# Kernel tuning notes

Measured on AMD Instinct MI355X. Metric: run time of the kernel, lower is better.

The kernel has to match this reference:

```python
import jax, jax.numpy as jnp
import numpy as np

N_NODES = 50000
IN_CH, HID_CH, OUT_CH = 128, 128, 64
N_EDGES = 800000


def setup_inputs() -> dict:
    key = jax.random.key(0)
    k = jax.random.split(key, 6)
    x = jax.random.normal(k[0], (N_NODES, IN_CH), dtype=jnp.float32)
    edge_index = jax.random.randint(k[1], (2, N_EDGES), 0, N_NODES, dtype=jnp.int64)
    # Glorot-ish init for weights
    W1 = jax.random.normal(k[2], (IN_CH, HID_CH), dtype=jnp.float32) * (1.0 / np.sqrt(IN_CH))
    b1 = jnp.zeros((HID_CH,), dtype=jnp.float32)
    W2 = jax.random.normal(k[3], (HID_CH, OUT_CH), dtype=jnp.float32) * (1.0 / np.sqrt(HID_CH))
    b2 = jnp.zeros((OUT_CH,), dtype=jnp.float32)
    return {"x": x, "edge_index": edge_index, "W1": W1, "b1": b1, "W2": W2, "b2": b2}


def _gcn_conv(x, src, dst, W, b, n_nodes):
    """PyG GCNConv: linear, add self-loops, symmetric deg^-1/2 normalization, scatter-add."""
    h = x @ W  # [N, F_out]
    loop = jnp.arange(n_nodes, dtype=src.dtype)
    s = jnp.concatenate([src, loop])  # [E+N]
    d = jnp.concatenate([dst, loop])
    # in-degree on target nodes (including self-loops), edge weight = 1
    deg = jnp.zeros((n_nodes,), dtype=h.dtype).at[d].add(1.0)
    dinv = jnp.where(deg > 0, jax.lax.rsqrt(deg), 0.0)
    norm = dinv[s] * dinv[d]  # [E+N]
    msg = h[s] * norm[:, None]  # [E+N, F_out]
    out = jax.ops.segment_sum(msg, d, num_segments=n_nodes)
    return out + b


def reference(x, edge_index, W1, b1, W2, b2):
    src, dst = edge_index[0], edge_index[1]
    h = _gcn_conv(x, src, dst, W1, b1, N_NODES)
    h = jax.nn.relu(h)
    # dropout in eval mode -> identity
    out = _gcn_conv(h, src, dst, W2, b2, N_NODES)
    return out
```

## Files before the change

kernel.cpp:

```cpp
#include <hip/hip_runtime.h>

typedef __attribute__((ext_vector_type(8))) short bf16x8;
typedef __attribute__((ext_vector_type(4))) float f32x4;

constexpr int NN = 50000;
constexpr int NE = 800000;
constexpr int C1 = 128;
constexpr int C2 = 64;
constexpr int NBK = 196;
constexpr int EPB = 2048;
constexpr int NBLK = (NE + EPB - 1) / EPB;
constexpr int MT = NN / 16;
constexpr int CAP = 8192;
constexpr int GB = (NN + 3) / 4;
constexpr int MMB = 500;
constexpr int MMWAVES = MMB * 4;

constexpr int K1G = 1024;
constexpr int MM1_NW = (K1G - NBLK) * 4;

__device__ __forceinline__ unsigned short f2bf(float f) {
    unsigned int u = __float_as_uint(f);
    u += 0x7FFFu + ((u >> 16) & 1u);
    return (unsigned short)(u >> 16);
}
__device__ __forceinline__ float2 bf2f(unsigned int u) {
    return make_float2(__uint_as_float(u << 16), __uint_as_float(u & 0xFFFF0000u));
}
__device__ __forceinline__ unsigned int pk2(float a, float b) {
    return (unsigned int)f2bf(a) | ((unsigned int)f2bf(b) << 16);
}
__device__ __forceinline__ bf16x8 pack8(float4 a, float4 b) {
    bf16x8 r;
    r[0] = (short)f2bf(a.x); r[1] = (short)f2bf(a.y);
    r[2] = (short)f2bf(a.z); r[3] = (short)f2bf(a.w);
    r[4] = (short)f2bf(b.x); r[5] = (short)f2bf(b.y);
    r[6] = (short)f2bf(b.z); r[7] = (short)f2bf(b.w);
    return r;
}

struct BinSmem {
    int lhist[NBK];
    int ls[256];
    int lcur[NBK];
    unsigned int lbuf[EPB];
};

__device__ void bin_work(const int* __restrict__ src, const int* __restrict__ dst,
                         unsigned int* __restrict__ ebuf, int* __restrict__ localOff,
                         BinSmem& S) {
    const int t = threadIdx.x;
    const int base = blockIdx.x * EPB;
    if (t < NBK) S.lhist[t] = 0;
    __syncthreads();
    int b[8]; unsigned int p[8];
    #pragma unroll
    for (int i = 0; i < 8; i++) {
        int e = base + i * 256 + t;
        if (e < NE) {
            int s = src[e], d = dst[e];
            b[i] = d >> 8;
            p[i] = ((unsigned int)(d & 255) << 16) | (unsigned int)s;
            atomicAdd(&S.lhist[b[i]], 1);
        } else b[i] = -1;
    }
    __syncthreads();
    int v = (t < NBK) ? S.lhist[t] : 0;
    S.ls[t] = v;
    __syncthreads();
    #pragma unroll
    for (int d = 1; d < 256; d <<= 1) {
        int u = (t >= d) ? S.ls[t - d] : 0;
        __syncthreads();
        S.ls[t] += u;
        __syncthreads();
    }
    if (t < NBK) {
        S.lcur[t] = S.ls[t] - v;
        localOff[blockIdx.x * 200 + t] = S.ls[t] - v;
    }
    if (t == NBK - 1) localOff[blockIdx.x * 200 + NBK] = S.ls[t];
    __syncthreads();
    #pragma unroll
    for (int i = 0; i < 8; i++) {
        if (b[i] >= 0) {
            int lp = atomicAdd(&S.lcur[b[i]], 1);
            S.lbuf[lp] = p[i];
        }
    }
    __syncthreads();
    #pragma unroll
    for (int i = 0; i < 8; i++)
        ebuf[base + i * 256 + t] = S.lbuf[i * 256 + t];
}

__device__ void mm1_work(const float* __restrict__ x, const float* __restrict__ W,
                         unsigned short* __restrict__ g1,
                         unsigned short (&wl)[4][8][64][8]) {
    const int t = threadIdx.x;
    for (int i = 0; i < 64; i++) {
        int idx = i * 256 + t;
        int k = idx >> 7, n = idx & 127;
        wl[k >> 5][n >> 4][((k >> 3) & 3) * 16 + (n & 15)][k & 7] = f2bf(W[idx]);
    }
    __syncthreads();
    const int lane = t & 63, lm = lane & 15, quad = lane >> 4;

    bf16x8 bfr[4][8];
    #pragma unroll
    for (int s = 0; s < 4; s++)
        #pragma unroll
        for (int nt = 0; nt < 8; nt++)
            bfr[s][nt] = *(const bf16x8*)&wl[s][nt][lane][0];

    const int widx = (blockIdx.x - NBLK) * 4 + (t >> 6);
    for (int tile = widx; tile < MT; tile += MM1_NW) {
        int row0 = tile << 4;
        const float* xr = x + (size_t)(row0 + lm) * 128 + quad * 8;
        bf16x8 af[4];
        #pragma unroll
        for (int s = 0; s < 4; s++) {
            float4 p = *(const float4*)(xr + s * 32);
            float4 q = *(const float4*)(xr + s * 32 + 4);
            af[s] = pack8(p, q);
        }
        f32x4 acc[8];
        #pragma unroll
        for (int nt = 0; nt < 8; nt++) acc[nt] = (f32x4){0.f, 0.f, 0.f, 0.f};
        #pragma unroll
        for (int s = 0; s < 4; s++)
            #pragma unroll
            for (int nt = 0; nt < 8; nt++)
                acc[nt] = __builtin_amdgcn_mfma_f32_16x16x32_bf16(af[s], bfr[s][nt],
                                                                  acc[nt], 0, 0, 0);
        #pragma unroll
        for (int nt = 0; nt < 8; nt++)
            #pragma unroll
            for (int r = 0; r < 4; r++)
                g1[(size_t)(row0 + quad * 4 + r) * 128 + nt * 16 + lm] = f2bf(acc[nt][r]);
    }
}

__global__ __launch_bounds__(256, 2) void k1_kernel(const int* __restrict__ src,
                                                    const int* __restrict__ dst,
                                                    unsigned int* __restrict__ ebuf,
                                                    int* __restrict__ localOff,
                                                    const float* __restrict__ x,
                                                    const float* __restrict__ W1,
                                                    unsigned short* __restrict__ g1) {
    __shared__ union { BinSmem b; unsigned short wl[4][8][64][8]; } sm;
    if (blockIdx.x < NBLK) bin_work(src, dst, ebuf, localOff, sm.b);
    else                   mm1_work(x, W1, g1, sm.wl);
}

__global__ __launch_bounds__(256) void place_kernel(const unsigned int* __restrict__ ebuf,
                                                    const int* __restrict__ localOff,
                                                    unsigned short* __restrict__ esrc,
                                                    int* __restrict__ cnt,
                                                    int* __restrict__ off,
                                                    float* __restrict__ dinv) {
    __shared__ unsigned int lbuf[CAP];
    __shared__ int lhist[256];
    __shared__ int ls[256];
    __shared__ int lcur[256];
    __shared__ int red[256];
    const int t = threadIdx.x;
    const int bkt = blockIdx.x;
    const int node0 = bkt << 8;
    const int nnodes = min(256, NN - node0);

    const int j0 = 2 * t, j1 = 2 * t + 1;
    int s0 = 0, l0 = 0, s1 = 0, l1 = 0;
    if (j0 < NBLK) { s0 = localOff[j0 * 200 + bkt]; l0 = localOff[j0 * 200 + bkt + 1] - s0; }
    if (j1 < NBLK) { s1 = localOff[j1 * 200 + bkt]; l1 = localOff[j1 * 200 + bkt + 1] - s1; }

    red[t] = s0 + s1;
    ls[t] = l0 + l1;
    lhist[t] = 0;
    __syncthreads();
    #pragma unroll
    for (int d = 1; d < 256; d <<= 1) {
        int u = (t >= d) ? ls[t - d] : 0;
        int r = (t + d < 256) ? red[t + d] : 0;
        __syncthreads();
        ls[t] += u;
        red[t] += r;
        __syncthreads();
    }
    const int segBase = red[0];
    const int total = ls[255];
    const int base0 = ls[t] - (l0 + l1);
    const int base1 = base0 + l0;
    const bool fits = (total <= CAP);

    if (fits) {
        const unsigned int* q0 = ebuf + j0 * EPB + s0;
        for (int k = 0; k < l0; k++) lbuf[base0 + k] = q0[k];
        const unsigned int* q1 = ebuf + j1 * EPB + s1;
        for (int k = 0; k < l1; k++) lbuf[base1 + k] = q1[k];
        __syncthreads();
        for (int k = t; k < total; k += 256) atomicAdd(&lhist[lbuf[k] >> 16], 1);
    } else {
        const unsigned int* q0 = ebuf + j0 * EPB + s0;
        for (int k = 0; k < l0; k++) atomicAdd(&lhist[q0[k] >> 16], 1);
        const unsigned int* q1 = ebuf + j1 * EPB + s1;
        for (int k = 0; k < l1; k++) atomicAdd(&lhist[q1[k] >> 16], 1);
    }
    __syncthreads();
    int v = lhist[t];
    ls[t] = v;
    __syncthreads();
    #pragma unroll
    for (int d = 1; d < 256; d <<= 1) {
        int u = (t >= d) ? ls[t - d] : 0;
        __syncthreads();
        ls[t] += u;
        __syncthreads();
    }
    int ex = ls[t] - v;
    lcur[t] = ex;
    if (t < nnodes) {
        cnt[node0 + t] = v;
        off[node0 + t] = segBase + ex;
        dinv[node0 + t] = rsqrtf((float)v + 1.0f);
    }
    __syncthreads();
    if (fits) {
        for (int k = t; k < total; k += 256) {
            unsigned int pp = lbuf[k];
            int lp = atomicAdd(&lcur[pp >> 16], 1);
            esrc[segBase + lp] = (unsigned short)(pp & 0xFFFFu);
        }
    } else {
        const unsigned int* q0 = ebuf + j0 * EPB + s0;
        for (int k = 0; k < l0; k++) {
            unsigned int pp = q0[k];
            int lp = atomicAdd(&lcur[pp >> 16], 1);
            esrc[segBase + lp] = (unsigned short)(pp & 0xFFFFu);
        }
        const unsigned int* q1 = ebuf + j1 * EPB + s1;
        for (int k = 0; k < l1; k++) {
            unsigned int pp = q1[k];
            int lp = atomicAdd(&lcur[pp >> 16], 1);
            esrc[segBase + lp] = (unsigned short)(pp & 0xFFFFu);
        }
    }
}

__global__ __launch_bounds__(256) void gather1_kernel(const unsigned short* __restrict__ g1,
                                                      const unsigned short* __restrict__ esrc,
                                                      const int* __restrict__ off,
                                                      const int* __restrict__ cnt,
                                                      const float* __restrict__ dinv,
                                                      const float* __restrict__ b1,
                                                      unsigned short* __restrict__ x2) {
    const int n = blockIdx.x * 4 + (threadIdx.x >> 6);
    if (n >= NN) return;
    const int lane = threadIdx.x & 63;
    const unsigned int* G = (const unsigned int*)g1;
    const float dn = dinv[n];
    float2 ps = bf2f(G[(size_t)n * 64 + lane]);
    float a0 = dn * ps.x, a1 = dn * ps.y;
    float c0 = 0.f, c1 = 0.f;
    const int s0 = off[n], c = cnt[n];
    for (int base = 0; base < c; base += 64) {
        const int m = min(64, c - base);
        int vidx = 0; float vdin = 0.f;
        if (lane < m) {
            vidx = esrc[s0 + base + lane];
            vdin = dinv[vidx];
        }
        int i = 0;
        for (; i + 3 < m; i += 4) {
            int sA = __shfl(vidx, i),     sB = __shfl(vidx, i + 1);
            int sC = __shfl(vidx, i + 2), sD = __shfl(vidx, i + 3);
            float dA = __shfl(vdin, i),     dB = __shfl(vdin, i + 1);
            float dC = __shfl(vdin, i + 2), dD = __shfl(vdin, i + 3);
            unsigned int vA = G[(size_t)sA * 64 + lane];
            unsigned int vB = G[(size_t)sB * 64 + lane];
            unsigned int vC = G[(size_t)sC * 64 + lane];
            unsigned int vD = G[(size_t)sD * 64 + lane];
            float2 pA = bf2f(vA); a0 = fmaf(dA, pA.x, a0); a1 = fmaf(dA, pA.y, a1);
            float2 pB = bf2f(vB); c0 = fmaf(dB, pB.x, c0); c1 = fmaf(dB, pB.y, c1);
            float2 pC = bf2f(vC); a0 = fmaf(dC, pC.x, a0); a1 = fmaf(dC, pC.y, a1);
            float2 pD = bf2f(vD); c0 = fmaf(dD, pD.x, c0); c1 = fmaf(dD, pD.y, c1);
        }
        for (; i < m; i++) {
            int sA = __shfl(vidx, i);
            float dA = __shfl(vdin, i);
            float2 pA = bf2f(G[(size_t)sA * 64 + lane]);
            a0 = fmaf(dA, pA.x, a0); a1 = fmaf(dA, pA.y, a1);
        }
    }
    a0 += c0; a1 += c1;
    const float2 bb = ((const float2*)b1)[lane];
    const float o0 = fmaxf(dn * a0 + bb.x, 0.f);
    const float o1 = fmaxf(dn * a1 + bb.y, 0.f);
    ((unsigned int*)x2)[(size_t)n * 64 + lane] = pk2(o0, o1);
}

__global__ __launch_bounds__(256, 2) void mm2_kernel(const unsigned short* __restrict__ x2,
                                                     const float* __restrict__ W,
                                                     const float* __restrict__ dinv,
                                                     unsigned short* __restrict__ g2) {
    __shared__ unsigned short wl[4][4][64][8];
    const int t = threadIdx.x;
    for (int i = 0; i < 32; i++) {
        int idx = i * 256 + t;
        int k = idx >> 6, n = idx & 63;
        wl[k >> 5][n >> 4][((k >> 3) & 3) * 16 + (n & 15)][k & 7] = f2bf(W[idx]);
    }
    __syncthreads();
    const int lane = t & 63, lm = lane & 15, quad = lane >> 4;

    bf16x8 bfr[4][4];
    #pragma unroll
    for (int s = 0; s < 4; s++)
        #pragma unroll
        for (int nt = 0; nt < 4; nt++)
            bfr[s][nt] = *(const bf16x8*)&wl[s][nt][lane][0];

    int wg = blockIdx.x * 4 + (t >> 6);
    for (int tile = wg; tile < MT; tile += MMWAVES) {
        int row0 = tile << 4;
        const bf16x8* xr = (const bf16x8*)(x2 + (size_t)(row0 + lm) * 128 + quad * 8);
        bf16x8 af[4];
        #pragma unroll
        for (int s = 0; s < 4; s++) af[s] = xr[s * 4];
        f32x4 acc[4];
        #pragma unroll
        for (int nt = 0; nt < 4; nt++) acc[nt] = (f32x4){0.f, 0.f, 0.f, 0.f};
        #pragma unroll
        for (int s = 0; s < 4; s++)
            #pragma unroll
            for (int nt = 0; nt < 4; nt++)
                acc[nt] = __builtin_amdgcn_mfma_f32_16x16x32_bf16(af[s], bfr[s][nt],
                                                                  acc[nt], 0, 0, 0);
        float4 dv = *(const float4*)(dinv + row0 + quad * 4);
        float dvv[4] = {dv.x, dv.y, dv.z, dv.w};
        #pragma unroll
        for (int nt = 0; nt < 4; nt++)
            #pragma unroll
            for (int r = 0; r < 4; r++)
                g2[(size_t)(row0 + quad * 4 + r) * 64 + nt * 16 + lm] =
                    f2bf(acc[nt][r] * dvv[r]);
    }
}

__global__ __launch_bounds__(256) void gather2_kernel(const unsigned short* __restrict__ g2,
                                                      const unsigned short* __restrict__ esrc,
                                                      const int* __restrict__ off,
                                                      const int* __restrict__ cnt,
                                                      const float* __restrict__ dinv,
                                                      const float* __restrict__ b2,
                                                      float* __restrict__ out) {
    const int n = blockIdx.x * 4 + (threadIdx.x >> 6);
    if (n >= NN) return;
    const int lane = threadIdx.x & 63;
    const unsigned short* G = g2;
    float a0 = __uint_as_float((unsigned int)G[(size_t)n * 64 + lane] << 16);
    float c0 = 0.f;
    const int s0 = off[n], c = cnt[n];
    for (int base = 0; base < c; base += 64) {
        const int m = min(64, c - base);
        int vidx = 0;
        if (lane < m) vidx = esrc[s0 + base + lane];
        int i = 0;
        for (; i + 3 < m; i += 4) {
            int sA = __shfl(vidx, i),     sB = __shfl(vidx, i + 1);
            int sC = __shfl(vidx, i + 2), sD = __shfl(vidx, i + 3);
            unsigned short vA = G[(size_t)sA * 64 + lane];
            unsigned short vB = G[(size_t)sB * 64 + lane];
            unsigned short vC = G[(size_t)sC * 64 + lane];
            unsigned short vD = G[(size_t)sD * 64 + lane];
            a0 += __uint_as_float((unsigned int)vA << 16);
            c0 += __uint_as_float((unsigned int)vB << 16);
            a0 += __uint_as_float((unsigned int)vC << 16);
            c0 += __uint_as_float((unsigned int)vD << 16);
        }
        for (; i < m; i++) {
            int sA = __shfl(vidx, i);
            a0 += __uint_as_float((unsigned int)G[(size_t)sA * 64 + lane] << 16);
        }
    }
    a0 += c0;
    out[(size_t)n * 64 + lane] = dinv[n] * a0 + b2[lane];
}

extern "C" void kernel_launch(void* const* d_in, const int* in_sizes, int n_in,
                              void* d_out, int out_size, void* d_ws, size_t ws_size,
                              hipStream_t stream) {
    const float* x  = (const float*)d_in[0];
    const int* edges = (const int*)d_in[1];
    const float* W1 = (const float*)d_in[2];
    const float* b1 = (const float*)d_in[3];
    const float* W2 = (const float*)d_in[4];
    const float* b2 = (const float*)d_in[5];
    const int* src = edges;
    const int* dst = edges + NE;

    int* localOff  = (int*)d_ws;
    unsigned int* ebuf = (unsigned int*)(localOff + 78208);
    unsigned short* esrc = (unsigned short*)(ebuf + (size_t)NBLK * EPB);
    int* cnt       = (int*)(esrc + 800768);
    int* off       = cnt + 50048;
    float* dinv    = (float*)(off + 50048);
    unsigned short* g1 = (unsigned short*)(dinv + 50048);
    unsigned short* x2 = g1 + (size_t)NN * C1;
    unsigned short* g2 = g1;
    float* out = (float*)d_out;

    k1_kernel<<<K1G, 256, 0, stream>>>(src, dst, ebuf, localOff, x, W1, g1);
    place_kernel<<<NBK, 256, 0, stream>>>(ebuf, localOff, esrc, cnt, off, dinv);
    gather1_kernel<<<GB, 256, 0, stream>>>(g1, esrc, off, cnt, dinv, b1, x2);
    mm2_kernel<<<MMB, 256, 0, stream>>>(x2, W2, dinv, g2);
    gather2_kernel<<<GB, 256, 0, stream>>>(g2, esrc, off, cnt, dinv, b2, out);
}
```

Baseline: 179.6 us.

## Split first GEMM across binning and placement kernels to overlap work

The first dense matmul (x@W1) is split into two tile ranges. The first 500 row tiles run alongside edge binning in k1, and the rest run alongside the placement/CSR build in a new fused k2 kernel. The k1 grid shrinks and the place kernel gains extra matmul blocks. The aim is to hide the single-bucket placement phase, which occupies only 196 blocks, behind useful GEMM work. The cost is load-balance risk across the two phases and a larger shared-memory union in k2, which may lower occupancy.

```diff
diff --git a/kernel.cpp b/kernel.cpp
--- a/kernel.cpp
+++ b/kernel.cpp
@@ -16,8 +16,11 @@
 constexpr int MMB = 500;
 constexpr int MMWAVES = MMB * 4;
 
-constexpr int K1G = 1024;
-constexpr int MM1_NW = (K1G - NBLK) * 4;
+constexpr int T1 = 500;
+constexpr int K1G = 512;
+constexpr int MM1_NW_A = (K1G - NBLK) * 4;
+constexpr int K2G = 853;
+constexpr int MM1_NW_B = (K2G - NBK) * 4;
 
 __device__ __forceinline__ unsigned short f2bf(float f) {
     unsigned int u = __float_as_uint(f);
@@ -44,6 +47,13 @@
     int ls[256];
     int lcur[NBK];
     unsigned int lbuf[EPB];
+};
+struct PlaceSmem {
+    unsigned int lbuf[CAP];
+    int lhist[256];
+    int ls[256];
+    int lcur[256];
+    int red[256];
 };
 
 __device__ void bin_work(const int* __restrict__ src, const int* __restrict__ dst,
@@ -96,7 +106,8 @@
 
 __device__ void mm1_work(const float* __restrict__ x, const float* __restrict__ W,
                          unsigned short* __restrict__ g1,
-                         unsigned short (&wl)[4][8][64][8]) {
+                         unsigned short (&wl)[4][8][64][8],
+                         int mblk, int nwaves, int tile0, int tile1) {
     const int t = threadIdx.x;
     for (int i = 0; i < 64; i++) {
         int idx = i * 256 + t;
@@ -113,8 +124,8 @@
         for (int nt = 0; nt < 8; nt++)
             bfr[s][nt] = *(const bf16x8*)&wl[s][nt][lane][0];
 
-    const int widx = (blockIdx.x - NBLK) * 4 + (t >> 6);
-    for (int tile = widx; tile < MT; tile += MM1_NW) {
+    const int widx = mblk * 4 + (t >> 6);
+    for (int tile = tile0 + widx; tile < tile1; tile += nwaves) {
         int row0 = tile << 4;
         const float* xr = x + (size_t)(row0 + lm) * 128 + quad * 8;
         bf16x8 af[4];
@@ -138,6 +149,96 @@
             #pragma unroll
             for (int r = 0; r < 4; r++)
                 g1[(size_t)(row0 + quad * 4 + r) * 128 + nt * 16 + lm] = f2bf(acc[nt][r]);
+    }
+}
+
+__device__ void place_work(const unsigned int* __restrict__ ebuf,
+                           const int* __restrict__ localOff,
+                           unsigned short* __restrict__ esrc,
+                           int* __restrict__ cnt,
+                           int* __restrict__ off,
+                           float* __restrict__ dinv,
+                           PlaceSmem& S) {
+    const int t = threadIdx.x;
+    const int bkt = blockIdx.x;
+    const int node0 = bkt << 8;
+    const int nnodes = min(256, NN - node0);
+
+    const int j0 = 2 * t, j1 = 2 * t + 1;
+    int s0 = 0, l0 = 0, s1 = 0, l1 = 0;
+    if (j0 < NBLK) { s0 = localOff[j0 * 200 + bkt]; l0 = localOff[j0 * 200 + bkt + 1] - s0; }
+    if (j1 < NBLK) { s1 = localOff[j1 * 200 + bkt]; l1 = localOff[j1 * 200 + bkt + 1] - s1; }
+
+    S.red[t] = s0 + s1;
+    S.ls[t] = l0 + l1;
+    S.lhist[t] = 0;
+    __syncthreads();
+    #pragma unroll
+    for (int d = 1; d < 256; d <<= 1) {
+        int u = (t >= d) ? S.ls[t - d] : 0;
+        int r = (t + d < 256) ? S.red[t + d] : 0;
+        __syncthreads();
+        S.ls[t] += u;
+        S.red[t] += r;
+        __syncthreads();
+    }
+    const int segBase = S.red[0];
+    const int total = S.ls[255];
+    const int base0 = S.ls[t] - (l0 + l1);
+    const int base1 = base0 + l0;
+    const bool fits = (total <= CAP);
+
+    if (fits) {
+        const unsigned int* q0 = ebuf + j0 * EPB + s0;
+        for (int k = 0; k < l0; k++) S.lbuf[base0 + k] = q0[k];
+        const unsigned int* q1 = ebuf + j1 * EPB + s1;
+        for (int k = 0; k < l1; k++) S.lbuf[base1 + k] = q1[k];
+        __syncthreads();
+        for (int k = t; k < total; k += 256) atomicAdd(&S.lhist[S.lbuf[k] >> 16], 1);
+    } else {
+        const unsigned int* q0 = ebuf + j0 * EPB + s0;
+        for (int k = 0; k < l0; k++) atomicAdd(&S.lhist[q0[k] >> 16], 1);
+        const unsigned int* q1 = ebuf + j1 * EPB + s1;
+        for (int k = 0; k < l1; k++) atomicAdd(&S.lhist[q1[k] >> 16], 1);
+    }
+    __syncthreads();
+    int v = S.lhist[t];
+    S.ls[t] = v;
+    __syncthreads();
+    #pragma unroll
+    for (int d = 1; d < 256; d <<= 1) {
+        int u = (t >= d) ? S.ls[t - d] : 0;
+        __syncthreads();
+        S.ls[t] += u;
+        __syncthreads();
+    }
+    int ex = S.ls[t] - v;
+    S.lcur[t] = ex;
+    if (t < nnodes) {
+        cnt[node0 + t] = v;
+        off[node0 + t] = segBase + ex;
+        dinv[node0 + t] = rsqrtf((float)v + 1.0f);
+    }
+    __syncthreads();
+    if (fits) {
+        for (int k = t; k < total; k += 256) {
+            unsigned int pp = S.lbuf[k];
+            int lp = atomicAdd(&S.lcur[pp >> 16], 1);
+            esrc[segBase + lp] = (unsigned short)(pp & 0xFFFFu);
+        }
+    } else {
+        const unsigned int* q0 = ebuf + j0 * EPB + s0;
+        for (int k = 0; k < l0; k++) {
+            unsigned int pp = q0[k];
+            int lp = atomicAdd(&S.lcur[pp >> 16], 1);
+            esrc[segBase + lp] = (unsigned short)(pp & 0xFFFFu);
+        }
+        const unsigned int* q1 = ebuf + j1 * EPB + s1;
+        for (int k = 0; k < l1; k++) {
+            unsigned int pp = q1[k];
+            int lp = atomicAdd(&S.lcur[pp >> 16], 1);
+            esrc[segBase + lp] = (unsigned short)(pp & 0xFFFFu);
+        }
     }
 }
 
@@ -150,100 +251,24 @@
                                                     unsigned short* __restrict__ g1) {
     __shared__ union { BinSmem b; unsigned short wl[4][8][64][8]; } sm;
     if (blockIdx.x < NBLK) bin_work(src, dst, ebuf, localOff, sm.b);
-    else                   mm1_work(x, W1, g1, sm.wl);
-}
-
-__global__ __launch_bounds__(256) void place_kernel(const unsigned int* __restrict__ ebuf,
+    else mm1_work(x, W1, g1, sm.wl, blockIdx.x - NBLK, MM1_NW_A, 0, T1);
+}
+
+__global__ __launch_bounds__(256, 2) void k2_kernel(const unsigned int* __restrict__ ebuf,
                                                     const int* __restrict__ localOff,
                                                     unsigned short* __restrict__ esrc,
                                                     int* __restrict__ cnt,
                                                     int* __restrict__ off,
-                                                    float* __restrict__ dinv) {
-    __shared__ unsigned int lbuf[CAP];
-    __shared__ int lhist[256];
-    __shared__ int ls[256];
-    __shared__ int lcur[256];
-    __shared__ int red[256];
-    const int t = threadIdx.x;
-    const int bkt = blockIdx.x;
-    const int node0 = bkt << 8;
-    const int nnodes = min(256, NN - node0);
-
-    const int j0 = 2 * t, j1 = 2 * t + 1;
-    int s0 = 0, l0 = 0, s1 = 0, l1 = 0;
-    if (j0 < NBLK) { s0 = localOff[j0 * 200 + bkt]; l0 = localOff[j0 * 200 + bkt + 1] - s0; }
-    if (j1 < NBLK) { s1 = localOff[j1 * 200 + bkt]; l1 = localOff[j1 * 200 + bkt + 1] - s1; }
-
-    red[t] = s0 + s1;
-    ls[t] = l0 + l1;
-    lhist[t] = 0;
-    __syncthreads();
-    #pragma unroll
-    for (int d = 1; d < 256; d <<= 1) {
-        int u = (t >= d) ? ls[t - d] : 0;
-        int r = (t + d < 256) ? red[t + d] : 0;
-        __syncthreads();
-        ls[t] += u;
-        red[t] += r;
-        __syncthreads();
-    }
-    const int segBase = red[0];
-    const int total = ls[255];
-    const int base0 = ls[t] - (l0 + l1);
-    const int base1 = base0 + l0;
-    const bool fits = (total <= CAP);
-
-    if (fits) {
-        const unsigned int* q0 = ebuf + j0 * EPB + s0;
-        for (int k = 0; k < l0; k++) lbuf[base0 + k] = q0[k];
-        const unsigned int* q1 = ebuf + j1 * EPB + s1;
-        for (int k = 0; k < l1; k++) lbuf[base1 + k] = q1[k];
-        __syncthreads();
-        for (int k = t; k < total; k += 256) atomicAdd(&lhist[lbuf[k] >> 16], 1);
-    } else {
-        const unsigned int* q0 = ebuf + j0 * EPB + s0;
-        for (int k = 0; k < l0; k++) atomicAdd(&lhist[q0[k] >> 16], 1);
-        const unsigned int* q1 = ebuf + j1 * EPB + s1;
-        for (int k = 0; k < l1; k++) atomicAdd(&lhist[q1[k] >> 16], 1);
-    }
-    __syncthreads();
-    int v = lhist[t];
-    ls[t] = v;
-    __syncthreads();
-    #pragma unroll
-    for (int d = 1; d < 256; d <<= 1) {
-        int u = (t >= d) ? ls[t - d] : 0;
-        __syncthreads();
-        ls[t] += u;
-        __syncthreads();
-    }
-    int ex = ls[t] - v;
-    lcur[t] = ex;
-    if (t < nnodes) {
-        cnt[node0 + t] = v;
-        off[node0 + t] = segBase + ex;
-        dinv[node0 + t] = rsqrtf((float)v + 1.0f);
-    }
-    __syncthreads();
-    if (fits) {
-        for (int k = t; k < total; k += 256) {
-            unsigned int pp = lbuf[k];
-            int lp = atomicAdd(&lcur[pp >> 16], 1);
-            esrc[segBase + lp] = (unsigned short)(pp & 0xFFFFu);
-        }
-    } else {
-        const unsigned int* q0 = ebuf + j0 * EPB + s0;
-        for (int k = 0; k < l0; k++) {
-            unsigned int pp = q0[k];
-            int lp = atomicAdd(&lcur[pp >> 16], 1);
-            esrc[segBase + lp] = (unsigned short)(pp & 0xFFFFu);
-        }
-        const unsigned int* q1 = ebuf + j1 * EPB + s1;
-        for (int k = 0; k < l1; k++) {
-            unsigned int pp = q1[k];
-            int lp = atomicAdd(&lcur[pp >> 16], 1);
-            esrc[segBase + lp] = (unsigned short)(pp & 0xFFFFu);
-        }
+                                                    float* __restrict__ dinv,
+                                                    const float* __restrict__ x,
+                                                    const float* __restrict__ W1,
+                                                    unsigned short* __restrict__ g1) {
+    __shared__ union { PlaceSmem p; unsigned short wl[4][8][64][8]; } sm;
+    if (blockIdx.x < NBK) place_work(ebuf, localOff, esrc, cnt, off, dinv, sm.p);
+    else {
+        const int mblk = blockIdx.x - NBK;
+        if (T1 + mblk * 4 >= MT) return;
+        mm1_work(x, W1, g1, sm.wl, mblk, MM1_NW_B, T1, MT);
     }
 }
 
@@ -411,7 +436,7 @@
     float* out = (float*)d_out;
 
     k1_kernel<<<K1G, 256, 0, stream>>>(src, dst, ebuf, localOff, x, W1, g1);
-    place_kernel<<<NBK, 256, 0, stream>>>(ebuf, localOff, esrc, cnt, off, dinv);
+    k2_kernel<<<K2G, 256, 0, stream>>>(ebuf, localOff, esrc, cnt, off, dinv, x, W1, g1);
     gather1_kernel<<<GB, 256, 0, stream>>>(g1, esrc, off, cnt, dinv, b1, x2);
     mm2_kernel<<<MMB, 256, 0, stream>>>(x2, W2, dinv, g2);
     gather2_kernel<<<GB, 256, 0, stream>>>(g2, esrc, off, cnt, dinv, b2, out);
```

Result: slower. 195.3 us (+8.7%).
